# Kernel tuning notes

Measured on AMD Instinct MI355X. Metric: run time of the kernel, lower is better.

Reference implementation:

```python
import jax, jax.numpy as jnp
import numpy as np

N, D, K, NUM_PAIRS = 8192, 128, 128, 262144


def setup_inputs() -> dict:
    rng = np.random.default_rng(0)
    labels = rng.integers(0, K, size=N).astype(np.int32)
    # positive pairs: off-diagonal (i,j) with labels[i]==labels[j], same as
    # (diag_mask * match).nonzero() in torch; take a fixed deterministic prefix.
    match = labels[:, None] == labels[None, :]
    np.fill_diagonal(match, False)
    pi, pj = np.nonzero(match)
    assert pi.shape[0] >= NUM_PAIRS
    pos_idx = np.stack([pi[:NUM_PAIRS], pj[:NUM_PAIRS]], axis=1).astype(np.int32)
    # negative pairs: vectorized rejection sampling of (i,j) with labels differing
    neg_chunks, need = [], NUM_PAIRS
    while need > 0:
        cand = rng.integers(0, N, size=(2 * need, 2))
        ok = labels[cand[:, 0]] != labels[cand[:, 1]]
        cand = cand[ok][:need]
        neg_chunks.append(cand)
        need -= cand.shape[0]
    neg_idx = np.concatenate(neg_chunks, axis=0).astype(np.int32)
    key = jax.random.key(0)
    k1, k2 = jax.random.split(key)
    return {
        "Xemb": jax.random.normal(k1, (N, D), dtype=jnp.float32),
        "scores": jax.random.normal(k2, (N,), dtype=jnp.float32),  # unused by forward, kept for signature fidelity
        "h_bias": jnp.asarray(1.0, dtype=jnp.float32),
        "labels": jnp.asarray(labels),
        "pos_idx": jnp.asarray(pos_idx),
        "neg_idx": jnp.asarray(neg_idx),
    }


def reference(Xemb, scores, h_bias, labels, pos_idx, neg_idx):
    bias = jax.nn.softplus(h_bias)
    # positive pairs: squared euclidean distance
    dpos = Xemb[pos_idx[:, 0]] - Xemb[pos_idx[:, 1]]          # [P, D]
    pos_distances_sq = jnp.sum(dpos * dpos, axis=1)           # [P]
    # negative pairs: euclidean distance with margin (softplus bias)
    dneg = Xemb[neg_idx[:, 0]] - Xemb[neg_idx[:, 1]]          # [P, D]
    neg_distances = jnp.sqrt(jnp.sum(dneg * dneg, axis=1))    # [P]
    pos_loss = 0.5 * jnp.mean(pos_distances_sq)
    neg_loss = 0.5 * jnp.mean(jax.nn.relu(bias - neg_distances) ** 2)
    return jnp.stack([pos_loss, neg_loss])  # (cont_pos, cont_neg)
```

## Files before the change

kernel.cpp:

```cpp
#include <hip/hip_runtime.h>
#include <math.h>

#define NPAIRS  262144
#define D4      32
#define TPB     256
#define NBLK    2048
#define GPB     (TPB / 32)
#define NGROUPS (NBLK * GPB)
#define PPG     (NPAIRS / NGROUPS)

__global__ __launch_bounds__(TPB, 4) void pair_kernel(
    const float* __restrict__ X,
    const int*   __restrict__ pos_i,
    const int*   __restrict__ neg_i,
    const float* __restrict__ h_bias,
    float* __restrict__ partials)
{
    const int lane  = threadIdx.x & 31;
    const int group = threadIdx.x >> 5;
    const int gid   = (blockIdx.x * TPB + threadIdx.x) >> 5;

    const float4* __restrict__ X4 = (const float4*)X;

    const float hb   = h_bias[0];
    const float bias = fmaxf(hb, 0.0f) + log1pf(expf(-fabsf(hb)));

    const int pidx = pos_i[gid * 32 + lane];
    const int nidx = neg_i[gid * 32 + lane];

    float posAcc = 0.0f;
    #pragma unroll
    for (int t = 0; t < PPG; ++t) {
        const int i = __shfl(pidx, 2 * t,     32);
        const int j = __shfl(pidx, 2 * t + 1, 32);
        const float4 a = X4[i * D4 + lane];
        const float4 b = X4[j * D4 + lane];
        float d;
        d = a.x - b.x; posAcc = fmaf(d, d, posAcc);
        d = a.y - b.y; posAcc = fmaf(d, d, posAcc);
        d = a.z - b.z; posAcc = fmaf(d, d, posAcc);
        d = a.w - b.w; posAcc = fmaf(d, d, posAcc);
    }

    float negAcc = 0.0f;
    #pragma unroll
    for (int t = 0; t < PPG; ++t) {
        const int i = __shfl(nidx, 2 * t,     32);
        const int j = __shfl(nidx, 2 * t + 1, 32);
        const float4 a = X4[i * D4 + lane];
        const float4 b = X4[j * D4 + lane];
        float d, s = 0.0f;
        d = a.x - b.x; s = fmaf(d, d, s);
        d = a.y - b.y; s = fmaf(d, d, s);
        d = a.z - b.z; s = fmaf(d, d, s);
        d = a.w - b.w; s = fmaf(d, d, s);
        #pragma unroll
        for (int m = 16; m > 0; m >>= 1) s += __shfl_xor(s, m, 32);
        const float r = fmaxf(bias - sqrtf(s), 0.0f);
        negAcc = fmaf(r, r, negAcc);
    }

    #pragma unroll
    for (int m = 16; m > 0; m >>= 1) posAcc += __shfl_xor(posAcc, m, 32);

    __shared__ float sp[GPB], sn[GPB];
    if (lane == 0) { sp[group] = posAcc; sn[group] = negAcc; }
    __syncthreads();
    if (threadIdx.x == 0) {
        float P = 0.f, Nn = 0.f;
        #pragma unroll
        for (int g = 0; g < GPB; ++g) { P += sp[g]; Nn += sn[g]; }
        partials[2 * blockIdx.x]     = P;
        partials[2 * blockIdx.x + 1] = Nn;
    }
}

__global__ __launch_bounds__(TPB) void finalize_kernel(
    const float* __restrict__ partials, float* __restrict__ out)
{
    __shared__ float sp[TPB], sn[TPB];
    float p = 0.0f, n = 0.0f;
    for (int b = threadIdx.x; b < NBLK; b += TPB) {
        p += partials[2 * b];
        n += partials[2 * b + 1];
    }
    sp[threadIdx.x] = p; sn[threadIdx.x] = n;
    __syncthreads();
    for (int s = TPB / 2; s > 0; s >>= 1) {
        if ((int)threadIdx.x < s) {
            sp[threadIdx.x] += sp[threadIdx.x + s];
            sn[threadIdx.x] += sn[threadIdx.x + s];
        }
        __syncthreads();
    }
    if (threadIdx.x == 0) {
        out[0] = 0.5f * sp[0] / (float)NPAIRS;
        out[1] = 0.5f * sn[0] / (float)NPAIRS;
    }
}

extern "C" void kernel_launch(void* const* d_in, const int* in_sizes, int n_in,
                              void* d_out, int out_size, void* d_ws, size_t ws_size,
                              hipStream_t stream) {
    const float* X      = (const float*)d_in[0];
    const float* h_bias = (const float*)d_in[2];
    const int*   pos_i  = (const int*)d_in[4];
    const int*   neg_i  = (const int*)d_in[5];
    float*       out    = (float*)d_out;
    float*       partials = (float*)d_ws;

    pair_kernel<<<NBLK, TPB, 0, stream>>>(X, pos_i, neg_i, h_bias, partials);
    finalize_kernel<<<1, TPB, 0, stream>>>(partials, out);
}
```

Baseline: 89.72 us.

## Double pairs per group, load index pairs as int2, transpose-reduce negative sums

Halves the block count so each 32-lane group handles 32 pairs instead of 16, and loads each (i,j) index pair as one int2. The per-pair butterfly reduction of negative distances is replaced by a recursive-halving transpose reduction, so after log2(32) exchange steps each lane holds one pair's full sum. This cuts cross-lane shuffles from five per pair to about one per pair, at the cost of a 32-entry register array and fewer resident blocks.

```diff
diff --git a/kernel.cpp b/kernel.cpp
--- a/kernel.cpp
+++ b/kernel.cpp
@@ -4,15 +4,15 @@
 #define NPAIRS  262144
 #define D4      32
 #define TPB     256
-#define NBLK    2048
+#define NBLK    1024
 #define GPB     (TPB / 32)
 #define NGROUPS (NBLK * GPB)
 #define PPG     (NPAIRS / NGROUPS)
 
 __global__ __launch_bounds__(TPB, 4) void pair_kernel(
     const float* __restrict__ X,
-    const int*   __restrict__ pos_i,
-    const int*   __restrict__ neg_i,
+    const int2*  __restrict__ pos_p,
+    const int2*  __restrict__ neg_p,
     const float* __restrict__ h_bias,
     float* __restrict__ partials)
 {
@@ -25,14 +25,14 @@
     const float hb   = h_bias[0];
     const float bias = fmaxf(hb, 0.0f) + log1pf(expf(-fabsf(hb)));
 
-    const int pidx = pos_i[gid * 32 + lane];
-    const int nidx = neg_i[gid * 32 + lane];
+    const int2 pp = pos_p[gid * 32 + lane];
+    const int2 np = neg_p[gid * 32 + lane];
 
     float posAcc = 0.0f;
     #pragma unroll
     for (int t = 0; t < PPG; ++t) {
-        const int i = __shfl(pidx, 2 * t,     32);
-        const int j = __shfl(pidx, 2 * t + 1, 32);
+        const int i = __shfl(pp.x, t, 32);
+        const int j = __shfl(pp.y, t, 32);
         const float4 a = X4[i * D4 + lane];
         const float4 b = X4[j * D4 + lane];
         float d;
@@ -41,27 +41,56 @@
         d = a.z - b.z; posAcc = fmaf(d, d, posAcc);
         d = a.w - b.w; posAcc = fmaf(d, d, posAcc);
     }
+    #pragma unroll
+    for (int m = 16; m > 0; m >>= 1) posAcc += __shfl_xor(posAcc, m, 32);
 
-    float negAcc = 0.0f;
+    float s[PPG];
     #pragma unroll
     for (int t = 0; t < PPG; ++t) {
-        const int i = __shfl(nidx, 2 * t,     32);
-        const int j = __shfl(nidx, 2 * t + 1, 32);
+        const int i = __shfl(np.x, t, 32);
+        const int j = __shfl(np.y, t, 32);
         const float4 a = X4[i * D4 + lane];
         const float4 b = X4[j * D4 + lane];
-        float d, s = 0.0f;
-        d = a.x - b.x; s = fmaf(d, d, s);
-        d = a.y - b.y; s = fmaf(d, d, s);
-        d = a.z - b.z; s = fmaf(d, d, s);
-        d = a.w - b.w; s = fmaf(d, d, s);
-        #pragma unroll
-        for (int m = 16; m > 0; m >>= 1) s += __shfl_xor(s, m, 32);
-        const float r = fmaxf(bias - sqrtf(s), 0.0f);
-        negAcc = fmaf(r, r, negAcc);
+        float d, acc = 0.0f;
+        d = a.x - b.x; acc = fmaf(d, d, acc);
+        d = a.y - b.y; acc = fmaf(d, d, acc);
+        d = a.z - b.z; acc = fmaf(d, d, acc);
+        d = a.w - b.w; acc = fmaf(d, d, acc);
+        s[t] = acc;
     }
-
     #pragma unroll
-    for (int m = 16; m > 0; m >>= 1) posAcc += __shfl_xor(posAcc, m, 32);
+    for (int t = 0; t < 16; ++t) {
+        const float send = (lane & 16) ? s[t]      : s[t + 16];
+        const float keep = (lane & 16) ? s[t + 16] : s[t];
+        s[t] = keep + __shfl_xor(send, 16, 32);
+    }
+    #pragma unroll
+    for (int t = 0; t < 8; ++t) {
+        const float send = (lane & 8) ? s[t]     : s[t + 8];
+        const float keep = (lane & 8) ? s[t + 8] : s[t];
+        s[t] = keep + __shfl_xor(send, 8, 32);
+    }
+    #pragma unroll
+    for (int t = 0; t < 4; ++t) {
+        const float send = (lane & 4) ? s[t]     : s[t + 4];
+        const float keep = (lane & 4) ? s[t + 4] : s[t];
+        s[t] = keep + __shfl_xor(send, 4, 32);
+    }
+    #pragma unroll
+    for (int t = 0; t < 2; ++t) {
+        const float send = (lane & 2) ? s[t]     : s[t + 2];
+        const float keep = (lane & 2) ? s[t + 2] : s[t];
+        s[t] = keep + __shfl_xor(send, 2, 32);
+    }
+    {
+        const float send = (lane & 1) ? s[0] : s[1];
+        const float keep = (lane & 1) ? s[1] : s[0];
+        s[0] = keep + __shfl_xor(send, 1, 32);
+    }
+    const float r = fmaxf(bias - sqrtf(s[0]), 0.0f);
+    float negAcc = r * r;
+    #pragma unroll
+    for (int m = 16; m > 0; m >>= 1) negAcc += __shfl_xor(negAcc, m, 32);
 
     __shared__ float sp[GPB], sn[GPB];
     if (lane == 0) { sp[group] = posAcc; sn[group] = negAcc; }
@@ -104,11 +133,11 @@
                               hipStream_t stream) {
     const float* X      = (const float*)d_in[0];
     const float* h_bias = (const float*)d_in[2];
-    const int*   pos_i  = (const int*)d_in[4];
-    const int*   neg_i  = (const int*)d_in[5];
+    const int2*  pos_p  = (const int2*)d_in[4];
+    const int2*  neg_p  = (const int2*)d_in[5];
     float*       out    = (float*)d_out;
     float*       partials = (float*)d_ws;
 
-    pair_kernel<<<NBLK, TPB, 0, stream>>>(X, pos_i, neg_i, h_bias, partials);
+    pair_kernel<<<NBLK, TPB, 0, stream>>>(X, pos_p, neg_p, h_bias, partials);
     finalize_kernel<<<1, TPB, 0, stream>>>(partials, out);
 }
```

Measured after the change: 91.29 us. Within noise of the previous version (+1.7%).

## Skip reloading repeated positive-pair row and load index pairs as int2

Applied to the files above, without the earlier changes.

Positive pairs come from np.nonzero, so they are sorted by first index. The kernel now keeps the previously loaded row of X in registers and reloads it only when the first index changes, which roughly halves gathers for positive pairs. Index pairs are read as int2, and the launch-bounds occupancy hint rises from 4 to 6. The reuse relies on the sorted order of the test's positive pairs; correctness still holds for any order, but the saving depends on the input, and the divergent-looking branch is uniform per wave.

```diff
diff --git a/kernel.cpp b/kernel.cpp
--- a/kernel.cpp
+++ b/kernel.cpp
@@ -9,10 +9,10 @@
 #define NGROUPS (NBLK * GPB)
 #define PPG     (NPAIRS / NGROUPS)
 
-__global__ __launch_bounds__(TPB, 4) void pair_kernel(
+__global__ __launch_bounds__(TPB, 6) void pair_kernel(
     const float* __restrict__ X,
-    const int*   __restrict__ pos_i,
-    const int*   __restrict__ neg_i,
+    const int2*  __restrict__ pos_p,
+    const int2*  __restrict__ neg_p,
     const float* __restrict__ h_bias,
     float* __restrict__ partials)
 {
@@ -25,15 +25,17 @@
     const float hb   = h_bias[0];
     const float bias = fmaxf(hb, 0.0f) + log1pf(expf(-fabsf(hb)));
 
-    const int pidx = pos_i[gid * 32 + lane];
-    const int nidx = neg_i[gid * 32 + lane];
+    const int2 pp = pos_p[gid * PPG + (lane & (PPG - 1))];
+    const int2 np = neg_p[gid * PPG + (lane & (PPG - 1))];
 
     float posAcc = 0.0f;
+    float4 a = make_float4(0.f, 0.f, 0.f, 0.f);
+    int    cur = -1;
     #pragma unroll
     for (int t = 0; t < PPG; ++t) {
-        const int i = __shfl(pidx, 2 * t,     32);
-        const int j = __shfl(pidx, 2 * t + 1, 32);
-        const float4 a = X4[i * D4 + lane];
+        const int i = __shfl(pp.x, t, 32);
+        const int j = __shfl(pp.y, t, 32);
+        if (i != cur) { a = X4[i * D4 + lane]; cur = i; }
         const float4 b = X4[j * D4 + lane];
         float d;
         d = a.x - b.x; posAcc = fmaf(d, d, posAcc);
@@ -41,27 +43,26 @@
         d = a.z - b.z; posAcc = fmaf(d, d, posAcc);
         d = a.w - b.w; posAcc = fmaf(d, d, posAcc);
     }
+    #pragma unroll
+    for (int m = 16; m > 0; m >>= 1) posAcc += __shfl_xor(posAcc, m, 32);
 
     float negAcc = 0.0f;
     #pragma unroll
     for (int t = 0; t < PPG; ++t) {
-        const int i = __shfl(nidx, 2 * t,     32);
-        const int j = __shfl(nidx, 2 * t + 1, 32);
-        const float4 a = X4[i * D4 + lane];
-        const float4 b = X4[j * D4 + lane];
+        const int i = __shfl(np.x, t, 32);
+        const int j = __shfl(np.y, t, 32);
+        const float4 a2 = X4[i * D4 + lane];
+        const float4 b2 = X4[j * D4 + lane];
         float d, s = 0.0f;
-        d = a.x - b.x; s = fmaf(d, d, s);
-        d = a.y - b.y; s = fmaf(d, d, s);
-        d = a.z - b.z; s = fmaf(d, d, s);
-        d = a.w - b.w; s = fmaf(d, d, s);
+        d = a2.x - b2.x; s = fmaf(d, d, s);
+        d = a2.y - b2.y; s = fmaf(d, d, s);
+        d = a2.z - b2.z; s = fmaf(d, d, s);
+        d = a2.w - b2.w; s = fmaf(d, d, s);
         #pragma unroll
         for (int m = 16; m > 0; m >>= 1) s += __shfl_xor(s, m, 32);
         const float r = fmaxf(bias - sqrtf(s), 0.0f);
         negAcc = fmaf(r, r, negAcc);
     }
-
-    #pragma unroll
-    for (int m = 16; m > 0; m >>= 1) posAcc += __shfl_xor(posAcc, m, 32);
 
     __shared__ float sp[GPB], sn[GPB];
     if (lane == 0) { sp[group] = posAcc; sn[group] = negAcc; }
@@ -104,11 +105,11 @@
                               hipStream_t stream) {
     const float* X      = (const float*)d_in[0];
     const float* h_bias = (const float*)d_in[2];
-    const int*   pos_i  = (const int*)d_in[4];
-    const int*   neg_i  = (const int*)d_in[5];
+    const int2*  pos_p  = (const int2*)d_in[4];
+    const int2*  neg_p  = (const int2*)d_in[5];
     float*       out    = (float*)d_out;
     float*       partials = (float*)d_ws;
 
-    pair_kernel<<<NBLK, TPB, 0, stream>>>(X, pos_i, neg_i, h_bias, partials);
+    pair_kernel<<<NBLK, TPB, 0, stream>>>(X, pos_p, neg_p, h_bias, partials);
     finalize_kernel<<<1, TPB, 0, stream>>>(partials, out);
 }
```

New measurement: 146.9 us. 1.64x slower.
